# Optimization experiments

Hardware: AMD Instinct MI355X
Metric: run time of the kernel (lower is better)

## Reference

```python
import jax, jax.numpy as jnp
import numpy as np


def _scan_dir(x, Wih, Whh, b, reverse):
    # x: (B,T,D); Wih: (4H,D); Whh: (4H,H); b: (4H,)  (= b_ih+b_hh)
    B = x.shape[0]
    H = Whh.shape[1]
    xg = jnp.einsum('btd,gd->btg', x, Wih) + b          # (B,T,4H) precomputed input projections
    xg = jnp.swapaxes(xg, 0, 1)                          # (T,B,4H)

    def step(carry, g_t):
        h, c = carry
        g = g_t + h @ Whh.T
        i, f, gg, o = jnp.split(g, 4, axis=-1)           # PyTorch gate order: i,f,g,o
        c = jax.nn.sigmoid(f) * c + jax.nn.sigmoid(i) * jnp.tanh(gg)
        h = jax.nn.sigmoid(o) * jnp.tanh(c)
        return (h, c), h

    h0 = jnp.zeros((B, H), x.dtype)
    _, hs = jax.lax.scan(step, (h0, h0), xg, reverse=reverse)
    return jnp.swapaxes(hs, 0, 1)                        # (B,T,H), time order preserved


def _bilstm(x, Wih_f, Whh_f, b_f, Wih_b, Whh_b, b_b):
    out_f = _scan_dir(x, Wih_f, Whh_f, b_f, reverse=False)
    out_b = _scan_dir(x, Wih_b, Whh_b, b_b, reverse=True)
    return jnp.concatenate([out_f, out_b], axis=-1)      # (B,T,2H)


def setup_inputs() -> dict:
    key = jax.random.key(0)
    ks = iter(jax.random.split(key, 32))
    B, T = 1024, 128
    H1, H2 = 50, 150

    def p(shape, scale):
        return (jax.random.normal(next(ks), shape, dtype=jnp.float32) * scale)

    s1 = 1.0 / np.sqrt(H1)
    s2 = 1.0 / np.sqrt(H2)
    inp = {
        'x': jax.random.normal(next(ks), (B, 1, T), dtype=jnp.float32),
        'rrs': jax.random.normal(next(ks), (B, 4), dtype=jnp.float32),
        # layer 1: in_dim=1, H=50, bidirectional
        'l1_Wih_f': p((4 * H1, 1), s1), 'l1_Whh_f': p((4 * H1, H1), s1), 'l1_b_f': p((4 * H1,), s1),
        'l1_Wih_b': p((4 * H1, 1), s1), 'l1_Whh_b': p((4 * H1, H1), s1), 'l1_b_b': p((4 * H1,), s1),
        # layer 2: in_dim=100, H=150, bidirectional
        'l2_Wih_f': p((4 * H2, 2 * H1), s2), 'l2_Whh_f': p((4 * H2, H2), s2), 'l2_b_f': p((4 * H2,), s2),
        'l2_Wih_b': p((4 * H2, 2 * H1), s2), 'l2_Whh_b': p((4 * H2, H2), s2), 'l2_b_b': p((4 * H2,), s2),
        # heads
        'head_W': p((20, 2 * H2), 0.05), 'head_b': p((20,), 0.05),
        'pef1_W': p((10, 4), 0.05), 'pef1_b': p((10,), 0.05),
        'pef2_W': p((2, 10), 0.05), 'pef2_b': p((2,), 0.05),
        'fc_W': p((4, 30), 0.05), 'fc_b': p((4,), 0.05),
    }
    return inp


def reference(x, rrs,
              l1_Wih_f, l1_Whh_f, l1_b_f, l1_Wih_b, l1_Whh_b, l1_b_b,
              l2_Wih_f, l2_Whh_f, l2_b_f, l2_Wih_b, l2_Whh_b, l2_b_b,
              head_W, head_b, pef1_W, pef1_b, pef2_W, pef2_b, fc_W, fc_b):
    xt = jnp.transpose(x, (0, 2, 1))                     # (B,T,1)
    out1 = _bilstm(xt, l1_Wih_f, l1_Whh_f, l1_b_f, l1_Wih_b, l1_Whh_b, l1_b_b)   # (B,T,100)
    out2 = _bilstm(out1, l2_Wih_f, l2_Whh_f, l2_b_f, l2_Wih_b, l2_Whh_b, l2_b_b) # (B,T,300)
    net = out2[:, -1]                                    # (B,300)
    waveform_feat = jax.nn.leaky_relu(net @ head_W.T + head_b, 0.3)              # (B,20)
    pef = jax.nn.leaky_relu(rrs @ pef1_W.T + pef1_b, 0.3)                        # (B,10)
    pef_logits = pef @ pef2_W.T + pef2_b                                         # (B,2)
    feat = jnp.concatenate([waveform_feat, pef], axis=1)                         # (B,30)
    logits = feat @ fc_W.T + fc_b                                                # (B,4)
    return (waveform_feat, pef_logits, feat, logits)
```

## Files before the change

kernel.cpp:

```cpp
#include <hip/hip_runtime.h>


typedef unsigned short u16;
typedef unsigned int u32;
typedef float f32x4 __attribute__((ext_vector_type(4)));
typedef _Float16 f16x8 __attribute__((ext_vector_type(8)));
typedef short s16x8 __attribute__((ext_vector_type(8)));

#if __has_builtin(__builtin_amdgcn_mfma_f32_16x16x32_f16)
#define USE_F16 1
#else
#define USE_F16 0
#endif

#define B1 1024
#define TT 128

__device__ __forceinline__ u16 to_h(float x) {
#if USE_F16
    _Float16 h = (_Float16)x;
    return __builtin_bit_cast(u16, h);
#else
    u32 u = __builtin_bit_cast(u32, x);
    u32 r = u + 0x7FFFu + ((u >> 16) & 1u);
    return (u16)(r >> 16);
#endif
}
__device__ __forceinline__ float from_h(u16 s) {
#if USE_F16
    return (float)__builtin_bit_cast(_Float16, s);
#else
    u32 u = ((u32)s) << 16;
    return __builtin_bit_cast(float, u);
#endif
}

__device__ __forceinline__ f32x4 mfma16(uint4 a, uint4 b, f32x4 c) {
#if USE_F16
    return __builtin_amdgcn_mfma_f32_16x16x32_f16(
        __builtin_bit_cast(f16x8, a), __builtin_bit_cast(f16x8, b), c, 0, 0, 0);
#else
    return __builtin_amdgcn_mfma_f32_16x16x32_bf16(
        __builtin_bit_cast(s16x8, a), __builtin_bit_cast(s16x8, b), c, 0, 0, 0);
#endif
}

#define LOG2E 1.4426950408889634f
__device__ __forceinline__ float sigm(float x) {
    return __builtin_amdgcn_rcpf(1.f + __builtin_amdgcn_exp2f(-LOG2E * x));
}
__device__ __forceinline__ float tanh_(float x) {
    return 1.f - 2.f * __builtin_amdgcn_rcpf(1.f + __builtin_amdgcn_exp2f(2.f * LOG2E * x));
}
__device__ __forceinline__ float clampf(float x, float k) {
    return fminf(fmaxf(x, -k), k);
}

__device__ __forceinline__ float lstm_cell(float ig, float fg, float gg, float og,
                                           float& c)
{
    float ei = __builtin_amdgcn_exp2f(-LOG2E * ig);
    float ef = __builtin_amdgcn_exp2f(-LOG2E * fg);
    float eg = __builtin_amdgcn_exp2f(2.f * LOG2E * clampf(gg, 15.f));
    float P   = (1.f + ei) * (eg + 1.f);
    float num = fmaf(c, P, (eg - 1.f) * (1.f + ef));
    float cn  = num * __builtin_amdgcn_rcpf((1.f + ef) * P);
    c = cn;
    float eo = __builtin_amdgcn_exp2f(-LOG2E * og);
    float ec = __builtin_amdgcn_exp2f(2.f * LOG2E * clampf(cn, 15.f));
    return (ec - 1.f) * __builtin_amdgcn_rcpf((1.f + eo) * (ec + 1.f));
}

__device__ __forceinline__ void wg_barrier_lds() {
    __builtin_amdgcn_sched_barrier(0);
    asm volatile("s_waitcnt lgkmcnt(0)" ::: "memory");
    __builtin_amdgcn_s_barrier();
    __builtin_amdgcn_sched_barrier(0);
}

__device__ __forceinline__ void prep_frag_body(
    const float* __restrict__ Wih, const float* __restrict__ Whh,
    const float* __restrict__ bias, uint4* __restrict__ dst,
    int GR, int KT, int x_off, int x_len, int h_off, int h_len, int bias_k,
    int bid, int l)
{
    int tile = bid / KT, kt = bid - tile * KT;
    int ml = l & 15;
    int qq = ml >> 2, tau = ml & 3;
    int jj = tile * 4 + qq;
    bool valid = jj < GR;
    int row = tau * GR + jj;
    u32 dw[4];
    #pragma unroll
    for (int d = 0; d < 4; ++d) {
        u16 hh[2];
        #pragma unroll
        for (int s = 0; s < 2; ++s) {
            int j = d * 2 + s;
            int k = kt * 32 + (l >> 4) * 8 + j;
            float val = 0.f;
            if (valid) {
                if (k >= x_off && k < x_off + x_len) val = Wih[row * x_len + (k - x_off)];
                else if (k >= h_off && k < h_off + h_len) val = Whh[row * h_len + (k - h_off)];
                else if (k == bias_k) val = bias[row];
            }
            hh[s] = to_h(val);
        }
        dw[d] = (u32)hh[0] | ((u32)hh[1] << 16);
    }
    uint4 o; o.x = dw[0]; o.y = dw[1]; o.z = dw[2]; o.w = dw[3];
    dst[bid * 64 + l] = o;
}

__global__ void prep_all(const float* __restrict__ W1ihF, const float* __restrict__ W1hhF,
                         const float* __restrict__ b1F,
                         const float* __restrict__ W1ihB, const float* __restrict__ W1hhB,
                         const float* __restrict__ b1B,
                         const float* __restrict__ W2ihF, const float* __restrict__ W2hhF,
                         const float* __restrict__ b2F, const float* __restrict__ W2ihB,
                         uint4* __restrict__ frag1f, uint4* __restrict__ frag1b,
                         uint4* __restrict__ frag2f, float* __restrict__ WtT)
{
    int bid = blockIdx.x;
    int l = threadIdx.x;
    if (bid < 32)
        prep_frag_body(W1ihF, W1hhF, b1F, frag1f, 50, 2, 0, 1, 1, 50, 63, bid, l);
    else if (bid < 64)
        prep_frag_body(W1ihB, W1hhB, b1B, frag1b, 50, 2, 0, 1, 1, 50, 63, bid - 32, l);
    else if (bid < 384)
        prep_frag_body(W2ihF, W2hhF, b2F, frag2f, 150, 8, 0, 100, 100, 150, 255, bid - 64, l);
    else {
        int idx = (bid - 384) * 64 + l;
        if (idx < 60000) {
            int k = idx / 600, g = idx - k * 600;
            WtT[idx] = W2ihB[g * 100 + k];
        }
    }
}

__global__ __launch_bounds__(1024, 4) void l1_scan(
    const float* __restrict__ x, const uint4* __restrict__ fragF,
    const uint4* __restrict__ fragB, u16* __restrict__ out1f)
{
    const int tid = threadIdx.x;
    const int lane = tid & 63;
    const int w = tid >> 6;
    const int q = lane >> 4;
    const int b = lane & 15;
    const int blk = blockIdx.x;
    const int dir = blockIdx.y;
    const uint4* frag = dir ? fragB : fragF;

    __shared__ u16 v[2][1024];
    __shared__ float x_s[128][17];

    uint4 af0 = frag[(w * 2 + 0) * 64 + lane];
    uint4 af1 = frag[(w * 2 + 1) * 64 + lane];

    const int b0 = blk * 16;
    for (int idx = tid; idx < 1024; idx += 1024) ((u32*)v)[idx] = 0u;
    for (int idx = tid; idx < 2048; idx += 1024) {
        int bb = idx >> 7, t = idx & 127;
        x_s[t][bb] = x[(size_t)(b0 + bb) * TT + t];
    }
    __syncthreads();
    const u16 oneh = to_h(1.0f);
    if (tid < 16) {
        v[0][(112 + tid) * 8 + 7] = oneh;
        v[1][(112 + tid) * 8 + 7] = oneh;
        v[0][tid * 8] = to_h(x[(size_t)(b0 + tid) * TT + (dir ? TT - 1 : 0)]);
    }
    const int jj = w * 4 + q;
    const int k1 = 1 + jj;
    const int vslot = ((k1 >> 5) * 64 + ((k1 & 31) >> 3) * 16 + b) * 8 + (k1 & 7);
    const int k2 = dir * 50 + (jj < 50 ? jj : 0);
    const size_t eb = (((size_t)blk * 4 + (k2 >> 5)) * 64
                       + ((k2 & 31) >> 3) * 16 + b) * 8 + (k2 & 7);
    float c = 0.f;
    __syncthreads();

#define L1_STEP(T, CUR) { \
    uint4 bf0 = *(const uint4*)&v[CUR][lane * 8]; \
    uint4 bf1 = *(const uint4*)&v[CUR][(64 + lane) * 8]; \
    f32x4 acc = (f32x4){0.f, 0.f, 0.f, 0.f}; \
    acc = mfma16(af0, bf0, acc); \
    acc = mfma16(af1, bf1, acc); \
    const int tt = dir ? 127 - (T) : (T); \
    if (jj < 50) { \
        float hn = lstm_cell(acc[0], acc[1], acc[2], acc[3], c); \
        u16 hb = to_h(hn); \
        out1f[eb + (size_t)tt * 131072] = hb; \
        v[1 - (CUR)][vslot] = hb; \
    } \
    if (tid < 16 && (T) < 127) \
        v[1 - (CUR)][tid * 8] = to_h(x_s[dir ? 126 - (T) : (T) + 1][tid]); \
    wg_barrier_lds(); }

    for (int t2 = 0; t2 < TT; t2 += 2) {
        L1_STEP(t2, 0)
        L1_STEP(t2 + 1, 1)
    }
#undef L1_STEP
}

__global__ __launch_bounds__(512, 2) void l2f_scan(
    const uint4* __restrict__ frag, const u16* __restrict__ out1f,
    float* __restrict__ net)
{
    const int tid = threadIdx.x;
    const int lane = tid & 63;
    const int w = tid >> 6;
    const int q = lane >> 4;
    const int b = lane & 15;
    const int blk = blockIdx.x;
    const int b0 = blk * 16;
    const uint4* o4 = (const uint4*)out1f;

    __shared__ u16 v[2][4096];

    uint4 af[5][8];
    #pragma unroll
    for (int i = 0; i < 5; ++i)
        #pragma unroll
        for (int kt = 0; kt < 8; ++kt)
            af[i][kt] = frag[((w + 8 * i) * 8 + kt) * 64 + lane];

    for (int idx = tid; idx < 4096; idx += 512) ((u32*)v)[idx] = 0u;

    uint4 pf[4];
    #pragma unroll
    for (int ktx = 0; ktx < 4; ++ktx)
        pf[ktx] = o4[((size_t)blk * 4 + ktx) * 64 + lane];

    __syncthreads();
    const u16 oneh = to_h(1.0f);
    if (tid < 16) {
        v[0][(496 + tid) * 8 + 7] = oneh;
        v[1][(496 + tid) * 8 + 7] = oneh;
    }
    if (w == 0 && lane < 16) {
        uint2 xv; xv.x = pf[3].x; xv.y = pf[3].y;
        *(uint2*)&v[0][(192 + lane) * 8] = xv;
    }

    int vslot[5];
    #pragma unroll
    for (int p = 0; p < 5; ++p) {
        int jj = (w + 8 * p) * 4 + q;
        int k = 100 + (jj < 150 ? jj : 0);
        vslot[p] = ((k >> 5) * 64 + ((k & 31) >> 3) * 16 + b) * 8 + (k & 7);
    }
    float c[5] = {0.f, 0.f, 0.f, 0.f, 0.f};

    f32x4 acc[5];
    #pragma unroll
    for (int p = 0; p < 5; ++p) {
        acc[p] = mfma16(af[p][0], pf[0], (f32x4){0.f, 0.f, 0.f, 0.f});
        acc[p] = mfma16(af[p][1], pf[1], acc[p]);
        acc[p] = mfma16(af[p][2], pf[2], acc[p]);
    }
    __syncthreads();

#define L2F_STEP(T, CUR) { \
    uint4 bfu[5]; \
    _Pragma("unroll") for (int kh = 0; kh < 5; ++kh) \
        bfu[kh] = *(const uint4*)&v[CUR][((kh + 3) * 64 + lane) * 8]; \
    const int tn = ((T) < 127) ? (T) + 1 : 127; \
    _Pragma("unroll") for (int ktx = 0; ktx < 4; ++ktx) \
        pf[ktx] = o4[(((size_t)tn * 64 + blk) * 4 + ktx) * 64 + lane]; \
    _Pragma("unroll") for (int p = 0; p < 5; ++p) { \
        _Pragma("unroll") for (int kh = 0; kh < 5; ++kh) \
            acc[p] = mfma16(af[p][kh + 3], bfu[kh], acc[p]); \
        int jj = (w + 8 * p) * 4 + q; \
        if (jj < 150) { \
            float hn = lstm_cell(acc[p][0], acc[p][1], acc[p][2], acc[p][3], c[p]); \
            v[1 - (CUR)][vslot[p]] = to_h(hn); \
            if ((T) == 127) net[(size_t)(b0 + b) * 300 + jj] = hn; \
        } \
    } \
    _Pragma("unroll") for (int p = 0; p < 5; ++p) { \
        acc[p] = mfma16(af[p][0], pf[0], (f32x4){0.f, 0.f, 0.f, 0.f}); \
        acc[p] = mfma16(af[p][1], pf[1], acc[p]); \
        acc[p] = mfma16(af[p][2], pf[2], acc[p]); \
    } \
    if (w == 0 && lane < 16) { \
        uint2 xv; xv.x = pf[3].x; xv.y = pf[3].y; \
        *(uint2*)&v[1 - (CUR)][(192 + lane) * 8] = xv; \
    } \
    wg_barrier_lds(); }

    for (int t2 = 0; t2 < TT; t2 += 2) {
        L2F_STEP(t2, 0)
        L2F_STEP(t2 + 1, 1)
    }
#undef L2F_STEP
}

__global__ __launch_bounds__(640, 1) void l2b_step(
    const u16* __restrict__ out1f, const float* __restrict__ WtT,
    const float* __restrict__ bias, float* __restrict__ net)
{
    const int tid = threadIdx.x;
    const int blk = blockIdx.x;
    const int b0 = blk * 16;
    __shared__ alignas(16) float x_s[100][16];
    __shared__ alignas(16) float gbuf[16][644];
    for (int idx = tid; idx < 1600; idx += 640) {
        int k2 = idx >> 4, bb = idx & 15;
        x_s[k2][bb] = from_h(out1f[((((size_t)127 * 64 + blk) * 4 + (k2 >> 5)) * 64
                                    + ((k2 & 31) >> 3) * 16 + bb) * 8 + (k2 & 7)]);
    }
    __syncthreads();
    if (tid < 600) {
        int g = tid;
        float acc[16];
        #pragma unroll
        for (int bb = 0; bb < 16; ++bb) acc[bb] = 0.f;
        for (int k = 0; k < 100; ++k) {
            float wv = WtT[k * 600 + g];
            float4 xa = *(const float4*)&x_s[k][0];
            float4 xb = *(const float4*)&x_s[k][4];
            float4 xc = *(const float4*)&x_s[k][8];
            float4 xd = *(const float4*)&x_s[k][12];
            acc[0] = fmaf(wv, xa.x, acc[0]);  acc[1] = fmaf(wv, xa.y, acc[1]);
            acc[2] = fmaf(wv, xa.z, acc[2]);  acc[3] = fmaf(wv, xa.w, acc[3]);
            acc[4] = fmaf(wv, xb.x, acc[4]);  acc[5] = fmaf(wv, xb.y, acc[5]);
            acc[6] = fmaf(wv, xb.z, acc[6]);  acc[7] = fmaf(wv, xb.w, acc[7]);
            acc[8] = fmaf(wv, xc.x, acc[8]);  acc[9] = fmaf(wv, xc.y, acc[9]);
            acc[10] = fmaf(wv, xc.z, acc[10]); acc[11] = fmaf(wv, xc.w, acc[11]);
            acc[12] = fmaf(wv, xd.x, acc[12]); acc[13] = fmaf(wv, xd.y, acc[13]);
            acc[14] = fmaf(wv, xd.z, acc[14]); acc[15] = fmaf(wv, xd.w, acc[15]);
        }
        #pragma unroll
        for (int bb = 0; bb < 16; ++bb) gbuf[bb][g] = acc[bb];
    }
    __syncthreads();
    for (int idx = tid; idx < 2400; idx += 640) {
        int j = idx >> 4, bb = idx & 15;
        float ig = gbuf[bb][j]       + bias[j];
        float gg = gbuf[bb][j + 300] + bias[j + 300];
        float og = gbuf[bb][j + 450] + bias[j + 450];
        float cn = sigm(ig) * tanh_(gg);
        float hn = sigm(og) * tanh_(cn);
        net[(size_t)(b0 + bb) * 300 + 150 + j] = hn;
    }
}

__global__ void head1(const float* __restrict__ net, const float* __restrict__ rrs,
                      const float* __restrict__ headW, const float* __restrict__ headb,
                      const float* __restrict__ p1W, const float* __restrict__ p1b,
                      const float* __restrict__ p2W, const float* __restrict__ p2b,
                      float* __restrict__ out)
{
    int gid = blockIdx.x * 256 + threadIdx.x;
    int b = gid >> 2, og = gid & 3;
    float acc[5];
    #pragma unroll
    for (int o2 = 0; o2 < 5; ++o2) acc[o2] = headb[og * 5 + o2];
    const float* nb = net + (size_t)b * 300;
    for (int k = 0; k < 300; ++k) {
        float nv = nb[k];
        #pragma unroll
        for (int o2 = 0; o2 < 5; ++o2)
            acc[o2] = fmaf(headW[(og * 5 + o2) * 300 + k], nv, acc[o2]);
    }
    #pragma unroll
    for (int o2 = 0; o2 < 5; ++o2) {
        int o = og * 5 + o2;
        float vv = acc[o2] > 0.f ? acc[o2] : 0.3f * acc[o2];
        out[b * 20 + o] = vv;
        out[22528 + b * 30 + o] = vv;
    }
    if (og == 0) {
        float p[10];
        #pragma unroll
        for (int r = 0; r < 10; ++r) {
            float a = p1b[r];
            #pragma unroll
            for (int qq = 0; qq < 4; ++qq) a = fmaf(p1W[r * 4 + qq], rrs[b * 4 + qq], a);
            p[r] = a > 0.f ? a : 0.3f * a;
            out[22528 + b * 30 + 20 + r] = p[r];
        }
        #pragma unroll
        for (int s = 0; s < 2; ++s) {
            float a = p2b[s];
            #pragma unroll
            for (int r = 0; r < 10; ++r) a = fmaf(p2W[s * 10 + r], p[r], a);
            out[20480 + b * 2 + s] = a;
        }
    }
}

__global__ void head2(const float* __restrict__ fcW, const float* __restrict__ fcb,
                      float* __restrict__ out)
{
    int b = blockIdx.x * 256 + threadIdx.x;
    const float* feat = out + 22528 + b * 30;
    float f[30];
    #pragma unroll
    for (int k = 0; k < 30; ++k) f[k] = feat[k];
    #pragma unroll
    for (int s = 0; s < 4; ++s) {
        float a = fcb[s];
        #pragma unroll
        for (int k = 0; k < 30; ++k) a = fmaf(fcW[s * 30 + k], f[k], a);
        out[53248 + b * 4 + s] = a;
    }
}

extern "C" void kernel_launch(void* const* d_in, const int* in_sizes, int n_in,
                              void* d_out, int out_size, void* d_ws, size_t ws_size,
                              hipStream_t stream)
{
    const float* x     = (const float*)d_in[0];
    const float* rrs   = (const float*)d_in[1];
    const float* W1ihF = (const float*)d_in[2];
    const float* W1hhF = (const float*)d_in[3];
    const float* b1F   = (const float*)d_in[4];
    const float* W1ihB = (const float*)d_in[5];
    const float* W1hhB = (const float*)d_in[6];
    const float* b1B   = (const float*)d_in[7];
    const float* W2ihF = (const float*)d_in[8];
    const float* W2hhF = (const float*)d_in[9];
    const float* b2F   = (const float*)d_in[10];
    const float* W2ihB = (const float*)d_in[11];
    const float* b2B   = (const float*)d_in[13];
    const float* headW = (const float*)d_in[14];
    const float* headb = (const float*)d_in[15];
    const float* p1W   = (const float*)d_in[16];
    const float* p1b   = (const float*)d_in[17];
    const float* p2W   = (const float*)d_in[18];
    const float* p2b   = (const float*)d_in[19];
    const float* fcW   = (const float*)d_in[20];
    const float* fcb   = (const float*)d_in[21];
    float* out = (float*)d_out;

    char* ws = (char*)d_ws;
    uint4* frag1f = (uint4*)(ws + 0);
    uint4* frag1b = (uint4*)(ws + 32768);
    uint4* frag2f = (uint4*)(ws + 65536);
    float* WtT    = (float*)(ws + 393216);
    u16*   out1f  = (u16*)(ws + 655360);
    float* net    = (float*)(ws + 655360 + 33554432);
    (void)ws_size; (void)in_sizes; (void)n_in; (void)out_size;

    prep_all<<<1322, 64, 0, stream>>>(W1ihF, W1hhF, b1F, W1ihB, W1hhB, b1B,
                                      W2ihF, W2hhF, b2F, W2ihB,
                                      frag1f, frag1b, frag2f, WtT);
    l1_scan<<<dim3(64, 2), 1024, 0, stream>>>(x, frag1f, frag1b, out1f);
    l2f_scan<<<64, 512, 0, stream>>>(frag2f, out1f, net);
    l2b_step<<<64, 640, 0, stream>>>(out1f, WtT, b2B, net);
    head1<<<16, 256, 0, stream>>>(net, rrs, headW, headb, p1W, p1b, p2W, p2b, out);
    head2<<<4, 256, 0, stream>>>(fcW, fcb, out);
}
```

Before: 290.5 us.

## Halve l1_scan threads with two tiles per wave; double-buffer l2f input prefetch

The layer-1 scan now launches 512 threads instead of 1024, and each wave computes two gate tiles with two cell states, so per-step barriers synchronize fewer waves. The layer-2 forward scan keeps two prefetch register sets and loads the input fragments two steps ahead. It also moves the input-projection MFMAs to the start of each step, so they no longer sit after the cell update on the recurrent critical path. The cost is higher register pressure and more serial work per wave in l1.

```diff
diff --git a/kernel.cpp b/kernel.cpp
--- a/kernel.cpp
+++ b/kernel.cpp
@@ -138,7 +138,7 @@
     }
 }
 
-__global__ __launch_bounds__(1024, 4) void l1_scan(
+__global__ __launch_bounds__(512, 2) void l1_scan(
     const float* __restrict__ x, const uint4* __restrict__ fragF,
     const uint4* __restrict__ fragB, u16* __restrict__ out1f)
 {
@@ -154,12 +154,16 @@
     __shared__ u16 v[2][1024];
     __shared__ float x_s[128][17];
 
-    uint4 af0 = frag[(w * 2 + 0) * 64 + lane];
-    uint4 af1 = frag[(w * 2 + 1) * 64 + lane];
+    uint4 af[2][2];
+    #pragma unroll
+    for (int p = 0; p < 2; ++p)
+        #pragma unroll
+        for (int kt = 0; kt < 2; ++kt)
+            af[p][kt] = frag[((w + 8 * p) * 2 + kt) * 64 + lane];
 
     const int b0 = blk * 16;
-    for (int idx = tid; idx < 1024; idx += 1024) ((u32*)v)[idx] = 0u;
-    for (int idx = tid; idx < 2048; idx += 1024) {
+    for (int idx = tid; idx < 1024; idx += 512) ((u32*)v)[idx] = 0u;
+    for (int idx = tid; idx < 2048; idx += 512) {
         int bb = idx >> 7, t = idx & 127;
         x_s[t][bb] = x[(size_t)(b0 + bb) * TT + t];
     }
@@ -170,27 +174,36 @@
         v[1][(112 + tid) * 8 + 7] = oneh;
         v[0][tid * 8] = to_h(x[(size_t)(b0 + tid) * TT + (dir ? TT - 1 : 0)]);
     }
-    const int jj = w * 4 + q;
-    const int k1 = 1 + jj;
-    const int vslot = ((k1 >> 5) * 64 + ((k1 & 31) >> 3) * 16 + b) * 8 + (k1 & 7);
-    const int k2 = dir * 50 + (jj < 50 ? jj : 0);
-    const size_t eb = (((size_t)blk * 4 + (k2 >> 5)) * 64
-                       + ((k2 & 31) >> 3) * 16 + b) * 8 + (k2 & 7);
-    float c = 0.f;
+    int vslot[2]; size_t eb[2];
+    #pragma unroll
+    for (int p = 0; p < 2; ++p) {
+        int jj = (w + 8 * p) * 4 + q;
+        int k1 = 1 + (jj < 50 ? jj : 0);
+        vslot[p] = ((k1 >> 5) * 64 + ((k1 & 31) >> 3) * 16 + b) * 8 + (k1 & 7);
+        int k2 = dir * 50 + (jj < 50 ? jj : 0);
+        eb[p] = (((size_t)blk * 4 + (k2 >> 5)) * 64
+                 + ((k2 & 31) >> 3) * 16 + b) * 8 + (k2 & 7);
+    }
+    float c[2] = {0.f, 0.f};
     __syncthreads();
 
 #define L1_STEP(T, CUR) { \
     uint4 bf0 = *(const uint4*)&v[CUR][lane * 8]; \
     uint4 bf1 = *(const uint4*)&v[CUR][(64 + lane) * 8]; \
-    f32x4 acc = (f32x4){0.f, 0.f, 0.f, 0.f}; \
-    acc = mfma16(af0, bf0, acc); \
-    acc = mfma16(af1, bf1, acc); \
+    f32x4 acc[2]; \
+    _Pragma("unroll") for (int p = 0; p < 2; ++p) { \
+        acc[p] = mfma16(af[p][0], bf0, (f32x4){0.f, 0.f, 0.f, 0.f}); \
+        acc[p] = mfma16(af[p][1], bf1, acc[p]); \
+    } \
     const int tt = dir ? 127 - (T) : (T); \
-    if (jj < 50) { \
-        float hn = lstm_cell(acc[0], acc[1], acc[2], acc[3], c); \
-        u16 hb = to_h(hn); \
-        out1f[eb + (size_t)tt * 131072] = hb; \
-        v[1 - (CUR)][vslot] = hb; \
+    _Pragma("unroll") for (int p = 0; p < 2; ++p) { \
+        int jj = (w + 8 * p) * 4 + q; \
+        if (jj < 50) { \
+            float hn = lstm_cell(acc[p][0], acc[p][1], acc[p][2], acc[p][3], c[p]); \
+            u16 hb = to_h(hn); \
+            out1f[eb[p] + (size_t)tt * 131072] = hb; \
+            v[1 - (CUR)][vslot[p]] = hb; \
+        } \
     } \
     if (tid < 16 && (T) < 127) \
         v[1 - (CUR)][tid * 8] = to_h(x_s[dir ? 126 - (T) : (T) + 1][tid]); \
@@ -227,10 +240,12 @@
 
     for (int idx = tid; idx < 4096; idx += 512) ((u32*)v)[idx] = 0u;
 
-    uint4 pf[4];
-    #pragma unroll
-    for (int ktx = 0; ktx < 4; ++ktx)
-        pf[ktx] = o4[((size_t)blk * 4 + ktx) * 64 + lane];
+    uint4 pfA[4], pfB[4];
+    #pragma unroll
+    for (int ktx = 0; ktx < 4; ++ktx) {
+        pfA[ktx] = o4[((size_t)(0 * 64 + blk) * 4 + ktx) * 64 + lane];
+        pfB[ktx] = o4[((size_t)(1 * 64 + blk) * 4 + ktx) * 64 + lane];
+    }
 
     __syncthreads();
     const u16 oneh = to_h(1.0f);
@@ -239,7 +254,7 @@
         v[1][(496 + tid) * 8 + 7] = oneh;
     }
     if (w == 0 && lane < 16) {
-        uint2 xv; xv.x = pf[3].x; xv.y = pf[3].y;
+        uint2 xv; xv.x = pfA[3].x; xv.y = pfA[3].y;
         *(uint2*)&v[0][(192 + lane) * 8] = xv;
     }
 
@@ -251,26 +266,27 @@
         vslot[p] = ((k >> 5) * 64 + ((k & 31) >> 3) * 16 + b) * 8 + (k & 7);
     }
     float c[5] = {0.f, 0.f, 0.f, 0.f, 0.f};
-
-    f32x4 acc[5];
-    #pragma unroll
-    for (int p = 0; p < 5; ++p) {
-        acc[p] = mfma16(af[p][0], pf[0], (f32x4){0.f, 0.f, 0.f, 0.f});
-        acc[p] = mfma16(af[p][1], pf[1], acc[p]);
-        acc[p] = mfma16(af[p][2], pf[2], acc[p]);
-    }
-    __syncthreads();
-
-#define L2F_STEP(T, CUR) { \
+    __syncthreads();
+
+#define L2F_STEP(T, CUR, PFC, PFD) { \
     uint4 bfu[5]; \
     _Pragma("unroll") for (int kh = 0; kh < 5; ++kh) \
         bfu[kh] = *(const uint4*)&v[CUR][((kh + 3) * 64 + lane) * 8]; \
-    const int tn = ((T) < 127) ? (T) + 1 : 127; \
+    f32x4 acc[5]; \
+    _Pragma("unroll") for (int p = 0; p < 5; ++p) { \
+        acc[p] = mfma16(af[p][0], PFC[0], (f32x4){0.f, 0.f, 0.f, 0.f}); \
+        acc[p] = mfma16(af[p][1], PFC[1], acc[p]); \
+        acc[p] = mfma16(af[p][2], PFC[2], acc[p]); \
+    } \
+    const int tn = ((T) < 126) ? (T) + 2 : 127; \
     _Pragma("unroll") for (int ktx = 0; ktx < 4; ++ktx) \
-        pf[ktx] = o4[(((size_t)tn * 64 + blk) * 4 + ktx) * 64 + lane]; \
+        PFC[ktx] = o4[(((size_t)tn * 64 + blk) * 4 + ktx) * 64 + lane]; \
+    _Pragma("unroll") for (int kh = 0; kh < 4; ++kh) { \
+        _Pragma("unroll") for (int p = 0; p < 5; ++p) \
+            acc[p] = mfma16(af[p][kh + 3], bfu[kh], acc[p]); \
+    } \
     _Pragma("unroll") for (int p = 0; p < 5; ++p) { \
-        _Pragma("unroll") for (int kh = 0; kh < 5; ++kh) \
-            acc[p] = mfma16(af[p][kh + 3], bfu[kh], acc[p]); \
+        acc[p] = mfma16(af[p][7], bfu[4], acc[p]); \
         int jj = (w + 8 * p) * 4 + q; \
         if (jj < 150) { \
             float hn = lstm_cell(acc[p][0], acc[p][1], acc[p][2], acc[p][3], c[p]); \
@@ -278,20 +294,15 @@
             if ((T) == 127) net[(size_t)(b0 + b) * 300 + jj] = hn; \
         } \
     } \
-    _Pragma("unroll") for (int p = 0; p < 5; ++p) { \
-        acc[p] = mfma16(af[p][0], pf[0], (f32x4){0.f, 0.f, 0.f, 0.f}); \
-        acc[p] = mfma16(af[p][1], pf[1], acc[p]); \
-        acc[p] = mfma16(af[p][2], pf[2], acc[p]); \
-    } \
     if (w == 0 && lane < 16) { \
-        uint2 xv; xv.x = pf[3].x; xv.y = pf[3].y; \
+        uint2 xv; xv.x = PFD[3].x; xv.y = PFD[3].y; \
         *(uint2*)&v[1 - (CUR)][(192 + lane) * 8] = xv; \
     } \
     wg_barrier_lds(); }
 
     for (int t2 = 0; t2 < TT; t2 += 2) {
-        L2F_STEP(t2, 0)
-        L2F_STEP(t2 + 1, 1)
+        L2F_STEP(t2, 0, pfA, pfB)
+        L2F_STEP(t2 + 1, 1, pfB, pfA)
     }
 #undef L2F_STEP
 }
@@ -447,7 +458,7 @@
     prep_all<<<1322, 64, 0, stream>>>(W1ihF, W1hhF, b1F, W1ihB, W1hhB, b1B,
                                       W2ihF, W2hhF, b2F, W2ihB,
                                       frag1f, frag1b, frag2f, WtT);
-    l1_scan<<<dim3(64, 2), 1024, 0, stream>>>(x, frag1f, frag1b, out1f);
+    l1_scan<<<dim3(64, 2), 512, 0, stream>>>(x, frag1f, frag1b, out1f);
     l2f_scan<<<64, 512, 0, stream>>>(frag2f, out1f, net);
     l2b_step<<<64, 640, 0, stream>>>(out1f, WtT, b2B, net);
     head1<<<16, 256, 0, stream>>>(net, rrs, headW, headb, p1W, p1b, p2W, p2b, out);
```

Measured after the change: 280.8 us. 3.4% less time.
